# Optimization experiments

Measured on AMD Instinct MI355X. Metric: run time of the kernel, lower is better.

Reference implementation:

```python
import jax, jax.numpy as jnp
import numpy as np

B, S, DM = 2, 2048, 1024
H, D = 16, 64  # multiheads, head_dim; H*D == DM
NEG = -1e9


def setup_inputs() -> dict:
    key = jax.random.key(0)
    ks = jax.random.split(key, 7)
    xavier = float(np.sqrt(6.0 / (DM + H * D)))
    return {
        "Q": jax.random.normal(ks[0], (B, S, DM), dtype=jnp.float32),
        "K": jax.random.normal(ks[1], (B, S, DM), dtype=jnp.float32),
        "V": jax.random.normal(ks[2], (B, S, DM), dtype=jnp.float32),
        "V_len": jax.random.randint(ks[3], (B,), 0, S),
        "WQ": jax.random.uniform(ks[4], (DM, H * D), dtype=jnp.float32, minval=-xavier, maxval=xavier),
        "WK": jax.random.uniform(ks[5], (DM, H * D), dtype=jnp.float32, minval=-xavier, maxval=xavier),
        "WV": jax.random.uniform(ks[6], (DM, H * D), dtype=jnp.float32, minval=-xavier, maxval=xavier),
    }


def reference(Q, K, V, V_len, WQ, WK, WV):
    b, s, _ = Q.shape
    # project and split heads: [B,S,DM] -> [B,H,S,D]
    q = (Q @ WQ).reshape(b, s, H, D).transpose(0, 2, 1, 3)
    k = (K @ WK).reshape(b, s, H, D).transpose(0, 2, 1, 3)
    v = (V @ WV).reshape(b, s, H, D).transpose(0, 2, 1, 3)
    scores = jnp.einsum("bhqd,bhkd->bhqk", q, k) / jnp.sqrt(jnp.float32(D))
    # key padding mask: valid keys are positions < V_len[b]
    valid = jnp.arange(s)[None, :] < V_len[:, None]          # [B,S]
    scores = jnp.where(valid[:, None, None, :], scores, NEG)  # [B,H,Sq,Sk]
    attn = jax.nn.softmax(scores, axis=-1)
    out = jnp.einsum("bhqk,bhkd->bhqd", attn, v)
    return out.transpose(0, 2, 1, 3).reshape(b, s, H * D)
```

## Files before the change

### kernel.cpp

```cpp
#include <hip/hip_runtime.h>
#include <hip/hip_bf16.h>

#define NBATCH 2
#define SEQ 2048
#define DMODEL 1024
#define NHEAD 16
#define HDIM 64
#define ROWS (NBATCH*SEQ)

typedef __attribute__((ext_vector_type(8))) short bf16x8;
typedef __attribute__((ext_vector_type(4))) float f32x4;
typedef __attribute__((ext_vector_type(16))) float f32x16;

#define MFMA16 __builtin_amdgcn_mfma_f32_16x16x32_bf16
#define MFMA32 __builtin_amdgcn_mfma_f32_32x32x16_bf16

#define QSCALE 0.1803368801111204f
#define DEFER_THR 11.541560327111708f

static __device__ __forceinline__ unsigned short f2bf(float f) {
    unsigned int u = __float_as_uint(f);
    u += 0x7fffu + ((u >> 16) & 1u);
    return (unsigned short)(u >> 16);
}

static __device__ __forceinline__ unsigned cvtpk(float lo, float hi) {
    unsigned r;
    asm("v_cvt_pk_bf16_f32 %0, %1, %2" : "=v"(r) : "v"(lo), "v"(hi));
    return r;
}

static __device__ __forceinline__ void gld16(const unsigned short* g, unsigned short* l) {
    __builtin_amdgcn_global_load_lds(
        (const __attribute__((address_space(1))) unsigned int*)g,
        (__attribute__((address_space(3))) unsigned int*)l,
        16, 0, 0);
}

__global__ __launch_bounds__(256) void cvt_kernel(const float* __restrict__ Q, const float* __restrict__ K,
                                                  const float* __restrict__ V, const int* __restrict__ vlenp,
                                                  const float* __restrict__ W0, const float* __restrict__ W1,
                                                  const float* __restrict__ W2,
                                                  unsigned short* __restrict__ dq, unsigned short* __restrict__ dk,
                                                  unsigned short* __restrict__ dv,
                                                  unsigned short* __restrict__ T0, unsigned short* __restrict__ T1,
                                                  unsigned short* __restrict__ T2, int n8) {
    __shared__ float tile[64][65];
    const int z = blockIdx.z;
    const int tid = threadIdx.x;
    if (z == 3) {
        const int bx = blockIdx.x;
        if (bx >= 768) return;
        const int mat = bx >> 8, idx = bx & 255;
        const float* W = mat == 0 ? W0 : (mat == 1 ? W1 : W2);
        unsigned short* T = mat == 0 ? T0 : (mat == 1 ? T1 : T2);
        int rb = (idx >> 4) * 64, cb = (idx & 15) * 64;
        #pragma unroll
        for (int rep = 0; rep < 16; ++rep) {
            int i = rep * 256 + tid; int r = i >> 6, c = i & 63;
            tile[r][c] = W[(size_t)(rb + r) * DMODEL + cb + c];
        }
        __syncthreads();
        #pragma unroll
        for (int rep = 0; rep < 16; ++rep) {
            int i = rep * 256 + tid; int r = i >> 6, c = i & 63;
            T[(size_t)(cb + r) * DMODEL + rb + c] = f2bf(tile[c][r]);
        }
        return;
    }
    int i = blockIdx.x * 256 + tid;
    if (i >= n8) return;
    if (z) {
        int row = i >> 7;
        int bb = row >> 11, s = row & 2047;
        int vl = vlenp[bb];
        int lim = ((vl + 31) >> 5) << 5;
        if (z == 1) { if (vl == 0 || s >= lim) return; }
        else        { if (vl != 0 && s >= lim) return; }
    }
    const float* src = z == 0 ? Q : (z == 1 ? K : V);
    unsigned short* dst = z == 0 ? dq : (z == 1 ? dk : dv);
    const float4* s4 = (const float4*)src;
    float4 a = s4[2 * i], b = s4[2 * i + 1];
    union { bf16x8 v; unsigned short u[8]; } o;
    o.u[0] = f2bf(a.x); o.u[1] = f2bf(a.y); o.u[2] = f2bf(a.z); o.u[3] = f2bf(a.w);
    o.u[4] = f2bf(b.x); o.u[5] = f2bf(b.y); o.u[6] = f2bf(b.z); o.u[7] = f2bf(b.w);
    *(bf16x8*)(dst + (size_t)i * 8) = o.v;
}

__global__ __launch_bounds__(256) void proj_kernel(
        const unsigned short* __restrict__ Xq, const unsigned short* __restrict__ Xk,
        const unsigned short* __restrict__ Xv,
        const unsigned short* __restrict__ WTq, const unsigned short* __restrict__ WTk,
        const unsigned short* __restrict__ WTv, const int* __restrict__ vlenp,
        unsigned short* __restrict__ qp, unsigned short* __restrict__ kp,
        unsigned short* __restrict__ vtp) {
    const int mode = blockIdx.z;
    const int lin = blockIdx.y * gridDim.x + blockIdx.x;
    const int xcd = lin & 7, chunk = lin >> 3;
    const int by2 = xcd * 4 + (chunk >> 3);
    const int bx2 = chunk & 7;
    const int rowBase = by2 * 128;
    const int colBase = bx2 * 128;

    if (mode >= 1) {
        const int bb = rowBase >> 11, sS = rowBase & 2047;
        const int vl = vlenp[bb];
        const int lim = ((vl + 31) >> 5) << 5;
        if (mode == 1) { if (vl == 0 || sS >= lim) return; }
        else           { if (vl != 0 && sS >= lim) return; }
    }

    const unsigned short* X  = mode == 0 ? Xq  : (mode == 1 ? Xk  : Xv);
    const unsigned short* WT = mode == 0 ? WTq : (mode == 1 ? WTk : WTv);

    __shared__ unsigned short As[128 * 128];
    __shared__ unsigned short Bs[128 * 128];

    const int tid = threadIdx.x, lane = tid & 63, w = tid >> 6;
    const int wr = w >> 1, wc = w & 1;

    const int Xwave = (mode < 2) ? wr : wc;
    const int Wwave = (mode < 2) ? wc : wr;

    f32x4 acc[4][4];
    #pragma unroll
    for (int i = 0; i < 4; ++i)
        #pragma unroll
        for (int j = 0; j < 4; ++j) acc[i][j] = (f32x4){0.f, 0.f, 0.f, 0.f};

    const int rl4 = lane >> 4;
    const int gl  = lane & 15;

    for (int kt = 0; kt < DMODEL / 128; ++kt) {
        #pragma unroll
        for (int j = 0; j < 8; ++j) {
            int c = w * 8 + j;
            int r = c * 4 + rl4;
            int gg = gl ^ (r & 7);
            gld16(X  + (size_t)(rowBase + r) * DMODEL + kt * 128 + gg * 8, &As[c * 512]);
            gld16(WT + (size_t)(colBase + r) * DMODEL + kt * 128 + gg * 8, &Bs[c * 512]);
        }
        __syncthreads();
        #pragma unroll
        for (int ks = 0; ks < 4; ++ks) {
            const int kbyteNom = ks * 64 + ((lane >> 4) * 16);
            bf16x8 xf[4], wf[4];
            #pragma unroll
            for (int i = 0; i < 4; ++i) {
                int xr = Xwave * 64 + i * 16 + (lane & 15);
                xf[i] = *(const bf16x8*)((const char*)As + xr * 256 + (kbyteNom ^ ((xr & 7) << 4)));
                int wrow = Wwave * 64 + i * 16 + (lane & 15);
                wf[i] = *(const bf16x8*)((const char*)Bs + wrow * 256 + (kbyteNom ^ ((wrow & 7) << 4)));
            }
            if (mode < 2) {
                #pragma unroll
                for (int i = 0; i < 4; ++i)
                    #pragma unroll
                    for (int j = 0; j < 4; ++j)
                        acc[i][j] = MFMA16(xf[i], wf[j], acc[i][j], 0, 0, 0);
            } else {
                #pragma unroll
                for (int i = 0; i < 4; ++i)
                    #pragma unroll
                    for (int j = 0; j < 4; ++j)
                        acc[i][j] = MFMA16(wf[i], xf[j], acc[i][j], 0, 0, 0);
            }
        }
        __syncthreads();
    }

    if (mode < 2) {
        unsigned short* outp = (mode == 0) ? qp : kp;
        const float sc = (mode == 0) ? QSCALE : 1.0f;
        #pragma unroll
        for (int i = 0; i < 4; ++i)
            #pragma unroll
            for (int j = 0; j < 4; ++j)
                #pragma unroll
                for (int r = 0; r < 4; ++r) {
                    int grow = rowBase + wr * 64 + i * 16 + (lane >> 4) * 4 + r;
                    int gcol = colBase + wc * 64 + j * 16 + (lane & 15);
                    int b = grow >> 11, s = grow & 2047, hh = gcol >> 6, d = gcol & 63;
                    outp[((size_t)(b * NHEAD + hh) * SEQ + s) * HDIM + d] = f2bf(acc[i][j][r] * sc);
                }
    } else {
        #pragma unroll
        for (int i = 0; i < 4; ++i)
            #pragma unroll
            for (int j = 0; j < 4; ++j)
                #pragma unroll
                for (int r = 0; r < 4; ++r) {
                    int gcol = colBase + wr * 64 + i * 16 + (lane >> 4) * 4 + r;
                    int grow = rowBase + wc * 64 + j * 16 + (lane & 15);
                    int b = grow >> 11, s = grow & 2047, hh = gcol >> 6, d = gcol & 63;
                    vtp[((size_t)(b * NHEAD + hh) * HDIM + d) * SEQ + s] = f2bf(acc[i][j][r]);
                }
    }
}

__global__ __launch_bounds__(256, 4) void attn_kernel(
        const unsigned short* __restrict__ qp, const unsigned short* __restrict__ kp,
        const unsigned short* __restrict__ vtp, const int* __restrict__ vlenp,
        float* __restrict__ out) {
    const int tid = threadIdx.x, lane = tid & 63, w = tid >> 6;
    const int hh = lane >> 5;
    const int ql = lane & 31;
    const int qsub = w >> 1, kpar = w & 1;
    const int qt = blockIdx.x, h = blockIdx.y, b = blockIdx.z;
    const int vlen = vlenp[b];
    const int nt = (vlen == 0) ? (SEQ / 32) : ((vlen + 31) >> 5);
    const int myn = (nt - kpar + 1) >> 1;
    const int J = (nt + 1) >> 1;

    __shared__ unsigned short Kd[2][2][2048];
    __shared__ unsigned short Vd[2][2][2048];
    __shared__ float mlb[4][2][32];

    const size_t headQ = (size_t)(b * NHEAD + h) * SEQ * HDIM;
    const size_t headV = (size_t)(b * NHEAD + h) * HDIM * SEQ;

    const int qrow = qt * 64 + qsub * 32 + ql;
    bf16x8 qf[4];
    #pragma unroll
    for (int ks = 0; ks < 4; ++ks)
        qf[ks] = *(const bf16x8*)(qp + headQ + (size_t)qrow * HDIM + ks * 16 + hh * 8);

    f32x16 o0, o1;
    #pragma unroll
    for (int r = 0; r < 16; ++r) { o0[r] = 0.f; o1[r] = 0.f; }
    float m_run = -1e30f, l_run = 0.f;

    const int rloc = lane >> 3;
    const int ssw  = ((lane & 7) * 8) ^ (rloc * 8);
    const int gn   = (lane & 7) ^ rloc;
    const int koff = (gn & 3) * 8;
    const int dhi  = (gn >> 2) * 32;

    auto stageK = [&](int kvB, int buf) {
        #pragma unroll
        for (int c = 0; c < 4; ++c)
            gld16(kp + headQ + (size_t)(kvB + c * 8 + rloc) * HDIM + ssw, &Kd[kpar][buf][c * 512]);
    };
    auto stageV = [&](int kvB, int buf) {
        #pragma unroll
        for (int c = 0; c < 4; ++c)
            gld16(vtp + headV + (size_t)(c * 8 + rloc + dhi) * SEQ + kvB + koff, &Vd[kpar][buf][c * 512]);
    };

    if (myn > 0) { if (qsub == 0) stageK(kpar * 32, 0); else stageV(kpar * 32, 0); }

    for (int j = 0; j < J; ++j) {
        const int cur = j & 1;
        __syncthreads();

        if (j + 1 < myn) {
            const int nb = (kpar + 2 * (j + 1)) * 32;
            if (qsub == 0) stageK(nb, cur ^ 1); else stageV(nb, cur ^ 1);
        }

        if (j < myn) {
            const int kvBase = (kpar + 2 * j) * 32;
            const char* Kb = (const char*)&Kd[kpar][cur][0];
            const char* Vb = (const char*)&Vd[kpar][cur][0];

            f32x16 s0;
            #pragma unroll
            for (int r = 0; r < 16; ++r) s0[r] = 0.f;
            __builtin_amdgcn_s_setprio(1);
            #pragma unroll
            for (int ks = 0; ks < 4; ++ks) {
                const int kb = (ks * 32 + hh * 16) ^ ((ql & 7) << 4);
                bf16x8 kf = *(const bf16x8*)(Kb + ql * 128 + kb);
                s0 = MFMA32(kf, qf[ks], s0, 0, 0, 0);
            }
            __builtin_amdgcn_s_setprio(0);

            if (kvBase + 32 > vlen) {
                #pragma unroll
                for (int r = 0; r < 16; ++r) {
                    int kl = (r & 3) + 8 * (r >> 2) + 4 * hh;
                    if (kvBase + kl >= vlen) s0[r] = -1e9f;
                }
            }

            float mx[8];
            #pragma unroll
            for (int t = 0; t < 8; ++t) mx[t] = fmaxf(s0[t], s0[t + 8]);
            #pragma unroll
            for (int st = 4; st > 0; st >>= 1)
                #pragma unroll
                for (int t = 0; t < st; ++t) mx[t] = fmaxf(mx[t], mx[t + st]);
            float tmax = fmaxf(mx[0], __shfl_xor(mx[0], 32));

            if (!__all(tmax <= m_run + DEFER_THR)) {
                const float mnew = fmaxf(m_run, tmax);
                const float al = __builtin_amdgcn_exp2f(m_run - mnew);
                l_run *= al;
                #pragma unroll
                for (int r = 0; r < 16; ++r) { o0[r] *= al; o1[r] *= al; }
                m_run = mnew;
            }

            #pragma unroll
            for (int r = 0; r < 16; ++r) s0[r] = __builtin_amdgcn_exp2f(s0[r] - m_run);
            float sm[8];
            #pragma unroll
            for (int t = 0; t < 8; ++t) sm[t] = s0[t] + s0[t + 8];
            #pragma unroll
            for (int st = 4; st > 0; st >>= 1)
                #pragma unroll
                for (int t = 0; t < st; ++t) sm[t] += sm[t + st];
            l_run += sm[0] + __shfl_xor(sm[0], 32);

            unsigned d0[8];
            #pragma unroll
            for (int t = 0; t < 8; ++t) d0[t] = cvtpk(s0[2 * t], s0[2 * t + 1]);

            __builtin_amdgcn_s_setprio(1);
#define PV_SLICE(KSL)                                                              \
            {                                                                      \
                unsigned a0 = d0[4 * (KSL)],     b0 = d0[4 * (KSL) + 2];           \
                unsigned a1 = d0[4 * (KSL) + 1], b1 = d0[4 * (KSL) + 3];           \
                asm("v_permlane32_swap_b32 %0, %1" : "+v"(a0), "+v"(b0));          \
                asm("v_permlane32_swap_b32 %0, %1" : "+v"(a1), "+v"(b1));          \
                union { unsigned u[4]; bf16x8 v; } pa;                             \
                pa.u[0] = a0; pa.u[1] = a1; pa.u[2] = b0; pa.u[3] = b1;            \
                const int gA = 2 * (KSL) + hh;                                     \
                bf16x8 vfA = *(const bf16x8*)(Vb + ql * 128 + ((gA ^ (ql & 7)) << 4));        \
                bf16x8 vfB = *(const bf16x8*)(Vb + ql * 128 + (((4 + gA) ^ (ql & 7)) << 4));  \
                o0 = MFMA32(vfA, pa.v, o0, 0, 0, 0);                               \
                o1 = MFMA32(vfB, pa.v, o1, 0, 0, 0);                               \
            }
            PV_SLICE(0)
            PV_SLICE(1)
#undef PV_SLICE
            __builtin_amdgcn_s_setprio(0);
        }
    }

    if (hh == 0) { mlb[w][0][ql] = m_run; mlb[w][1][ql] = l_run; }
    __syncthreads();
    if (kpar == 1) {
        char* Ob = ((char*)Kd) + qsub * 8192;
        #pragma unroll
        for (int g = 0; g < 4; ++g) {
            int ad = ql * 256 + ((32 * g + 16 * hh) ^ (16 * (ql & 7)));
            *(float4*)(Ob + ad)       = make_float4(o0[4*g], o0[4*g+1], o0[4*g+2], o0[4*g+3]);
            *(float4*)(Ob + ad + 128) = make_float4(o1[4*g], o1[4*g+1], o1[4*g+2], o1[4*g+3]);
        }
    }
    __syncthreads();
    if (kpar == 0) {
        const float mp = mlb[w + 1][0][ql], lp = mlb[w + 1][1][ql];
        const float M = fmaxf(m_run, mp);
        const float a0 = __builtin_amdgcn_exp2f(m_run - M);
        const float a1 = __builtin_amdgcn_exp2f(mp - M);
        const float linv = 1.0f / (l_run * a0 + lp * a1);
        const char* Pb = ((const char*)Kd) + qsub * 8192;
        float* orow = out + (size_t)(b * SEQ + qrow) * DMODEL + h * HDIM;
        #pragma unroll
        for (int g = 0; g < 4; ++g) {
            int ad = ql * 256 + ((32 * g + 16 * hh) ^ (16 * (ql & 7)));
            float4 p0 = *(const float4*)(Pb + ad);
            float4 p1 = *(const float4*)(Pb + ad + 128);
            *(float4*)(orow + 8 * g + 4 * hh) = make_float4(
                (o0[4*g]   * a0 + p0.x * a1) * linv, (o0[4*g+1] * a0 + p0.y * a1) * linv,
                (o0[4*g+2] * a0 + p0.z * a1) * linv, (o0[4*g+3] * a0 + p0.w * a1) * linv);
            *(float4*)(orow + 32 + 8 * g + 4 * hh) = make_float4(
                (o1[4*g]   * a0 + p1.x * a1) * linv, (o1[4*g+1] * a0 + p1.y * a1) * linv,
                (o1[4*g+2] * a0 + p1.z * a1) * linv, (o1[4*g+3] * a0 + p1.w * a1) * linv);
        }
    }
}

extern "C" void kernel_launch(void* const* d_in, const int* in_sizes, int n_in,
                              void* d_out, int out_size, void* d_ws, size_t ws_size,
                              hipStream_t stream) {
    const float* Q  = (const float*)d_in[0];
    const float* K  = (const float*)d_in[1];
    const float* V  = (const float*)d_in[2];
    const int* V_len = (const int*)d_in[3];
    const float* WQ = (const float*)d_in[4];
    const float* WK = (const float*)d_in[5];
    const float* WV = (const float*)d_in[6];
    float* out = (float*)d_out;

    char* ws = (char*)d_ws;
    const size_t MB = 1024 * 1024;
    unsigned short* Xq  = (unsigned short*)(ws + 0 * MB);
    unsigned short* Xk  = (unsigned short*)(ws + 8 * MB);
    unsigned short* Xv  = (unsigned short*)(ws + 16 * MB);
    unsigned short* WTq = (unsigned short*)(ws + 24 * MB);
    unsigned short* WTk = (unsigned short*)(ws + 26 * MB);
    unsigned short* WTv = (unsigned short*)(ws + 28 * MB);
    unsigned short* qpj = (unsigned short*)(ws + 30 * MB);
    unsigned short* kpj = (unsigned short*)(ws + 38 * MB);
    unsigned short* vtp = (unsigned short*)(ws + 46 * MB);

    const int n8 = ROWS * DMODEL / 8;
    cvt_kernel<<<dim3((n8 + 255) / 256, 1, 4), 256, 0, stream>>>(
        Q, K, V, V_len, WQ, WK, WV, Xq, Xk, Xv, WTq, WTk, WTv, n8);
    proj_kernel<<<dim3(8, 32, 3), 256, 0, stream>>>(
        Xq, Xk, Xv, WTq, WTk, WTv, V_len, qpj, kpj, vtp);
    attn_kernel<<<dim3(SEQ / 64, NHEAD, NBATCH), 256, 0, stream>>>(qpj, kpj, vtp, V_len, out);
}
```

Before: 84.37 us.

## Use 8 waves per projection block with split-K LDS halves and new XCD mapping

The projection GEMM goes from 4 waves (each computing a 64x64 sub-tile) to 8 waves (each computing 64x32), which halves accumulator registers per wave and raises the number of waves available to hide latency. Shared memory is reorganized into two 64-wide k halves with a different XOR swizzle matching 128-byte rows. The block-to-XCD row mapping changes from contiguous row groups per XCD to interleaved rows. The tradeoffs are that each wave reloads the A fragments relative to its MFMA work, and the interleaving may reduce L2 locality per XCD.

After: 80.70 us. 1.05x faster.

```diff
diff --git a/kernel.cpp b/kernel.cpp
--- a/kernel.cpp
+++ b/kernel.cpp
@@ -88,7 +88,7 @@
     *(bf16x8*)(dst + (size_t)i * 8) = o.v;
 }
 
-__global__ __launch_bounds__(256) void proj_kernel(
+__global__ __launch_bounds__(512) void proj_kernel(
         const unsigned short* __restrict__ Xq, const unsigned short* __restrict__ Xk,
         const unsigned short* __restrict__ Xv,
         const unsigned short* __restrict__ WTq, const unsigned short* __restrict__ WTk,
@@ -98,7 +98,7 @@
     const int mode = blockIdx.z;
     const int lin = blockIdx.y * gridDim.x + blockIdx.x;
     const int xcd = lin & 7, chunk = lin >> 3;
-    const int by2 = xcd * 4 + (chunk >> 3);
+    const int by2 = (chunk >> 3) * 8 + xcd;
     const int bx2 = chunk & 7;
     const int rowBase = by2 * 128;
     const int colBase = bx2 * 128;
@@ -114,57 +114,56 @@
     const unsigned short* X  = mode == 0 ? Xq  : (mode == 1 ? Xk  : Xv);
     const unsigned short* WT = mode == 0 ? WTq : (mode == 1 ? WTk : WTv);
 
-    __shared__ unsigned short As[128 * 128];
-    __shared__ unsigned short Bs[128 * 128];
+    __shared__ unsigned short As[2][128 * 64];
+    __shared__ unsigned short Bs[2][128 * 64];
 
     const int tid = threadIdx.x, lane = tid & 63, w = tid >> 6;
-    const int wr = w >> 1, wc = w & 1;
-
-    const int Xwave = (mode < 2) ? wr : wc;
-    const int Wwave = (mode < 2) ? wc : wr;
-
-    f32x4 acc[4][4];
+    const int wr = w >> 2, wc = w & 3;
+
+    const int rloc = lane >> 3;
+    const int ssw  = ((lane & 7) * 8) ^ (rloc * 8);
+
+    f32x4 acc[4][2];
     #pragma unroll
     for (int i = 0; i < 4; ++i)
         #pragma unroll
-        for (int j = 0; j < 4; ++j) acc[i][j] = (f32x4){0.f, 0.f, 0.f, 0.f};
-
-    const int rl4 = lane >> 4;
-    const int gl  = lane & 15;
+        for (int j = 0; j < 2; ++j) acc[i][j] = (f32x4){0.f, 0.f, 0.f, 0.f};
 
     for (int kt = 0; kt < DMODEL / 128; ++kt) {
         #pragma unroll
-        for (int j = 0; j < 8; ++j) {
-            int c = w * 8 + j;
-            int r = c * 4 + rl4;
-            int gg = gl ^ (r & 7);
-            gld16(X  + (size_t)(rowBase + r) * DMODEL + kt * 128 + gg * 8, &As[c * 512]);
-            gld16(WT + (size_t)(colBase + r) * DMODEL + kt * 128 + gg * 8, &Bs[c * 512]);
-        }
+        for (int hf = 0; hf < 2; ++hf)
+            #pragma unroll
+            for (int j = 0; j < 2; ++j) {
+                int c = w * 2 + j;
+                int r = c * 8 + rloc;
+                gld16(X  + (size_t)(rowBase + r) * DMODEL + kt * 128 + hf * 64 + ssw, &As[hf][c * 512]);
+                gld16(WT + (size_t)(colBase + r) * DMODEL + kt * 128 + hf * 64 + ssw, &Bs[hf][c * 512]);
+            }
         __syncthreads();
-        #pragma unroll
-        for (int ks = 0; ks < 4; ++ks) {
-            const int kbyteNom = ks * 64 + ((lane >> 4) * 16);
-            bf16x8 xf[4], wf[4];
-            #pragma unroll
-            for (int i = 0; i < 4; ++i) {
-                int xr = Xwave * 64 + i * 16 + (lane & 15);
-                xf[i] = *(const bf16x8*)((const char*)As + xr * 256 + (kbyteNom ^ ((xr & 7) << 4)));
-                int wrow = Wwave * 64 + i * 16 + (lane & 15);
-                wf[i] = *(const bf16x8*)((const char*)Bs + wrow * 256 + (kbyteNom ^ ((wrow & 7) << 4)));
-            }
-            if (mode < 2) {
+
+        #pragma unroll
+        for (int hf = 0; hf < 2; ++hf) {
+            const char* Ab = (const char*)(mode < 2 ? &As[hf][0] : &Bs[hf][0]);
+            const char* Bb = (const char*)(mode < 2 ? &Bs[hf][0] : &As[hf][0]);
+            #pragma unroll
+            for (int ks = 0; ks < 2; ++ks) {
+                const int kbyte = ks * 64 + ((lane >> 4) * 16);
+                bf16x8 af[4], bfr[2];
+                #pragma unroll
+                for (int i = 0; i < 4; ++i) {
+                    int ar = wr * 64 + i * 16 + (lane & 15);
+                    af[i] = *(const bf16x8*)(Ab + ar * 128 + (kbyte ^ ((ar & 7) << 4)));
+                }
+                #pragma unroll
+                for (int j = 0; j < 2; ++j) {
+                    int br = wc * 32 + j * 16 + (lane & 15);
+                    bfr[j] = *(const bf16x8*)(Bb + br * 128 + (kbyte ^ ((br & 7) << 4)));
+                }
                 #pragma unroll
                 for (int i = 0; i < 4; ++i)
                     #pragma unroll
-                    for (int j = 0; j < 4; ++j)
-                        acc[i][j] = MFMA16(xf[i], wf[j], acc[i][j], 0, 0, 0);
-            } else {
-                #pragma unroll
-                for (int i = 0; i < 4; ++i)
-                    #pragma unroll
-                    for (int j = 0; j < 4; ++j)
-                        acc[i][j] = MFMA16(wf[i], xf[j], acc[i][j], 0, 0, 0);
+                    for (int j = 0; j < 2; ++j)
+                        acc[i][j] = MFMA16(af[i], bfr[j], acc[i][j], 0, 0, 0);
             }
         }
         __syncthreads();
@@ -176,11 +175,11 @@
         #pragma unroll
         for (int i = 0; i < 4; ++i)
             #pragma unroll
-            for (int j = 0; j < 4; ++j)
+            for (int j = 0; j < 2; ++j)
                 #pragma unroll
                 for (int r = 0; r < 4; ++r) {
                     int grow = rowBase + wr * 64 + i * 16 + (lane >> 4) * 4 + r;
-                    int gcol = colBase + wc * 64 + j * 16 + (lane & 15);
+                    int gcol = colBase + wc * 32 + j * 16 + (lane & 15);
                     int b = grow >> 11, s = grow & 2047, hh = gcol >> 6, d = gcol & 63;
                     outp[((size_t)(b * NHEAD + hh) * SEQ + s) * HDIM + d] = f2bf(acc[i][j][r] * sc);
                 }
@@ -188,11 +187,11 @@
         #pragma unroll
         for (int i = 0; i < 4; ++i)
             #pragma unroll
-            for (int j = 0; j < 4; ++j)
+            for (int j = 0; j < 2; ++j)
                 #pragma unroll
                 for (int r = 0; r < 4; ++r) {
                     int gcol = colBase + wr * 64 + i * 16 + (lane >> 4) * 4 + r;
-                    int grow = rowBase + wc * 64 + j * 16 + (lane & 15);
+                    int grow = rowBase + wc * 32 + j * 16 + (lane & 15);
                     int b = grow >> 11, s = grow & 2047, hh = gcol >> 6, d = gcol & 63;
                     vtp[((size_t)(b * NHEAD + hh) * HDIM + d) * SEQ + s] = f2bf(acc[i][j][r]);
                 }
@@ -401,7 +400,7 @@
     const int n8 = ROWS * DMODEL / 8;
     cvt_kernel<<<dim3((n8 + 255) / 256, 1, 4), 256, 0, stream>>>(
         Q, K, V, V_len, WQ, WK, WV, Xq, Xk, Xv, WTq, WTk, WTv, n8);
-    proj_kernel<<<dim3(8, 32, 3), 256, 0, stream>>>(
+    proj_kernel<<<dim3(8, 32, 3), 512, 0, stream>>>(
         Xq, Xk, Xv, WTq, WTk, WTv, V_len, qpj, kpj, vtp);
     attn_kernel<<<dim3(SEQ / 64, NHEAD, NBATCH), 256, 0, stream>>>(qpj, kpj, vtp, V_len, out);
 }
```
